# Performance work log

Measured on AMD Instinct MI355X. Metric: run time of the kernel, lower is better.

The kernel has to match this reference:

```python
import jax, jax.numpy as jnp
import numpy as np

B, S = 2, 2048          # batch, seq_len (tokens flattened to T=B*S)
HID = 2048              # hidden_size
H = 16                  # num_heads
DN, DR, DV = 128, 64, 128   # qk_nope_head_dim, qk_rope_head_dim, v_head_dim
QKD = DN + DR           # qk_head_dim = 192
QLR, KVR = 1536, 512    # q_lora_rank, kv_lora_rank
THETA = 10000.0
EPS = 1e-6
SCALE = QKD ** -0.5


def rmsnorm(x, w):
    return x * jax.lax.rsqrt(jnp.mean(x * x, axis=-1, keepdims=True) + EPS) * w


def rope_gptj(x, pos):
    # non-neox (interleaved / GPT-J) style on partial head dim DR
    # x: [T, Hx, DR], pos: [T]
    half = DR // 2
    inv_freq = 1.0 / (THETA ** (jnp.arange(half, dtype=jnp.float32) * 2.0 / DR))
    ang = pos.astype(jnp.float32)[:, None] * inv_freq[None, :]      # [T, half]
    cos = jnp.cos(ang)[:, None, :]
    sin = jnp.sin(ang)[:, None, :]
    x1 = x[..., 0::2]
    x2 = x[..., 1::2]
    o1 = x1 * cos - x2 * sin
    o2 = x2 * cos + x1 * sin
    return jnp.stack([o1, o2], axis=-1).reshape(x.shape)


def setup_inputs() -> dict:
    key = jax.random.key(0)
    ks = jax.random.split(key, 8)
    T = B * S
    positions = jnp.tile(jnp.arange(S, dtype=jnp.int64 if jax.config.jax_enable_x64 else jnp.int32), B)
    hidden_states = jax.random.normal(ks[0], (T, HID), dtype=jnp.float32)
    s = 0.02
    Wqa = jax.random.normal(ks[1], (HID, QLR), dtype=jnp.float32) * s
    q_a_ln_w = jnp.ones((QLR,), dtype=jnp.float32)
    Wqb = jax.random.normal(ks[2], (QLR, H * QKD), dtype=jnp.float32) * s
    Wkva = jax.random.normal(ks[3], (HID, KVR + DR), dtype=jnp.float32) * s
    kv_a_ln_w = jnp.ones((KVR,), dtype=jnp.float32)
    Wkvb = jax.random.normal(ks[4], (KVR, H * (DN + DV)), dtype=jnp.float32) * s
    Wo = jax.random.normal(ks[5], (H * DV, HID), dtype=jnp.float32) * s
    return {"positions": positions, "hidden_states": hidden_states, "Wqa": Wqa,
            "q_a_ln_w": q_a_ln_w, "Wqb": Wqb, "Wkva": Wkva,
            "kv_a_ln_w": kv_a_ln_w, "Wkvb": Wkvb, "Wo": Wo}


def reference(positions, hidden_states, Wqa, q_a_ln_w, Wqb, Wkva, kv_a_ln_w, Wkvb, Wo):
    T = hidden_states.shape[0]
    # --- Q path: low-rank compression ---
    ckq = hidden_states @ Wqa                       # [T, QLR]
    q_c = rmsnorm(ckq, q_a_ln_w)
    q = (q_c @ Wqb).reshape(T, H, QKD)              # [T, H, 192]
    q_nope, q_pe = q[..., :DN], q[..., DN:]
    # --- KV path: latent compression + shared rope key ---
    kv_no_split = hidden_states @ Wkva              # [T, KVR+DR]
    kv_c, k_pe = kv_no_split[:, :KVR], kv_no_split[:, KVR:]
    kv_c_normed = rmsnorm(kv_c, kv_a_ln_w)
    kv = (kv_c_normed @ Wkvb).reshape(T, H, DN + DV)
    k_nope, v = kv[..., :DN], kv[..., DN:]
    # --- RoPE on partial dims (non-neox) ---
    q_pe = rope_gptj(q_pe, positions)               # [T, H, DR]
    k_pe = rope_gptj(k_pe[:, None, :], positions)   # [T, 1, DR]
    # --- assemble full q/k per batch ---
    qf = jnp.concatenate([q_nope, q_pe], axis=-1).reshape(B, S, H, QKD)
    kf = jnp.concatenate([k_nope, jnp.broadcast_to(k_pe, (T, H, DR))], axis=-1).reshape(B, S, H, QKD)
    vf = v.reshape(B, S, H, DV)
    # --- causal attention ---
    scores = jnp.einsum('bqhd,bkhd->bhqk', qf, kf) * SCALE
    mask = jnp.tril(jnp.ones((S, S), dtype=bool))
    scores = jnp.where(mask[None, None], scores, jnp.finfo(scores.dtype).min)
    probs = jax.nn.softmax(scores, axis=-1)
    attn = jnp.einsum('bhqk,bkhd->bqhd', probs, vf).reshape(T, H * DV)
    # --- output projection ---
    return attn @ Wo                                # [T, HID]
```

## Files before the change

### kernel.cpp

```cpp
#include <hip/hip_runtime.h>
#include <hip/hip_bf16.h>

typedef __hip_bfloat16 bf16;
typedef short bf16x8 __attribute__((ext_vector_type(8)));
typedef float f32x4 __attribute__((ext_vector_type(4)));

#define MFMA16(a, b, c) __builtin_amdgcn_mfma_f32_16x16x32_bf16((a), (b), (c), 0, 0, 0)

__device__ __forceinline__ short f2bs(float f) {
  bf16 h = __float2bfloat16(f);
  return __builtin_bit_cast(short, h);
}
__device__ __forceinline__ float bs2f(short s) {
  return __bfloat162float(__builtin_bit_cast(bf16, s));
}

__device__ __forceinline__ void gload16(const void* g, const void* l) {
  __builtin_amdgcn_global_load_lds(
      (const __attribute__((address_space(1))) unsigned int*)g,
      (__attribute__((address_space(3))) unsigned int*)l, 16, 0, 0);
}

__device__ __forceinline__ void t_cvt_core(const float* __restrict__ src,
                                           bf16* __restrict__ dst, int K, int N,
                                           int bx, int by, short Ts[64][72]) {
  const long n0 = (long)bx * 64, k0 = (long)by * 64;
  const int r = threadIdx.x >> 2, c4 = threadIdx.x & 3;
  const float* s = src + (k0 + r) * (long)N + n0 + c4 * 16;
  #pragma unroll
  for (int j = 0; j < 4; ++j) {
    float4 v = *(const float4*)(s + j * 4);
    Ts[r][c4 * 16 + j * 4 + 0] = f2bs(v.x);
    Ts[r][c4 * 16 + j * 4 + 1] = f2bs(v.y);
    Ts[r][c4 * 16 + j * 4 + 2] = f2bs(v.z);
    Ts[r][c4 * 16 + j * 4 + 3] = f2bs(v.w);
  }
  __syncthreads();
  union { uint4 v; short sh[8]; } o0, o1;
  #pragma unroll
  for (int j = 0; j < 8; ++j) o0.sh[j] = Ts[c4 * 16 + j][r];
  #pragma unroll
  for (int j = 0; j < 8; ++j) o1.sh[j] = Ts[c4 * 16 + 8 + j][r];
  *(uint4*)(dst + (n0 + r) * (long)K + k0 + c4 * 16)     = o0.v;
  *(uint4*)(dst + (n0 + r) * (long)K + k0 + c4 * 16 + 8) = o1.v;
}

__global__ __launch_bounds__(256) void prep_all(
    const float* __restrict__ hs_f, bf16* __restrict__ hs_c,
    const float* __restrict__ qln_f, bf16* __restrict__ qln_c,
    const float* __restrict__ kvln_f, bf16* __restrict__ kvln_c,
    const float* __restrict__ Wqa_f, bf16* __restrict__ wqaT,
    const float* __restrict__ Wkva_f, bf16* __restrict__ wkvaT,
    const float* __restrict__ Wqb_f, bf16* __restrict__ wqbT,
    const float* __restrict__ Wkvb_f, bf16* __restrict__ wkvbT,
    const float* __restrict__ Wo_f, bf16* __restrict__ woT)
{
  __shared__ __align__(16) short Ts[64][72];
  const int bid = blockIdx.x;
  if (bid < 4097) {
    int i = bid * 256 + threadIdx.x;
    const float* s; bf16* d; int idx;
    if (i < 1048576)            { s = hs_f;   d = hs_c;   idx = i; }
    else if (i < 1048576 + 192) { s = qln_f;  d = qln_c;  idx = i - 1048576; }
    else                        { s = kvln_f; d = kvln_c; idx = i - 1048768; }
    const float4* sp = (const float4*)s;
    float4 a = sp[2 * idx], b = sp[2 * idx + 1];
    union { uint4 v; short sh[8]; } o;
    o.sh[0] = f2bs(a.x); o.sh[1] = f2bs(a.y); o.sh[2] = f2bs(a.z); o.sh[3] = f2bs(a.w);
    o.sh[4] = f2bs(b.x); o.sh[5] = f2bs(b.y); o.sh[6] = f2bs(b.z); o.sh[7] = f2bs(b.w);
    ((uint4*)d)[idx] = o.v;
  } else if (bid < 4865) {
    int l = bid - 4097;  t_cvt_core(Wqa_f, wqaT, 2048, 1536, l % 24, l / 24, Ts);
  } else if (bid < 5153) {
    int l = bid - 4865;  t_cvt_core(Wkva_f, wkvaT, 2048, 576, l % 9, l / 9, Ts);
  } else if (bid < 6305) {
    int l = bid - 5153;  t_cvt_core(Wqb_f, wqbT, 1536, 3072, l % 48, l / 48, Ts);
  } else if (bid < 6817) {
    int l = bid - 6305;  t_cvt_core(Wkvb_f, wkvbT, 512, 4096, l % 64, l / 64, Ts);
  } else {
    int l = bid - 6817;  t_cvt_core(Wo_f, woT, 2048, 2048, l % 32, l / 32, Ts);
  }
}

template<bool F32OUT>
__device__ __forceinline__ void gemm_core(
    short* As, short* Bs,
    const bf16* __restrict__ A, const bf16* __restrict__ BT, void* __restrict__ Cv,
    int N, int K, int lda, int ldb, int ldc, bf16* __restrict__ C2, int ncut,
    int nx, int nwg, int lin)
{
  const int tid = threadIdx.x, lane = tid & 63, w = tid >> 6;
  const int l15 = lane & 15, l4 = lane >> 4;
  const int wr = w >> 1, wc = w & 1;
  const int sl = (lin & 7) * (nwg >> 3) + (lin >> 3);
  const long bm = (long)(sl / nx) * 128, bn = (long)(sl % nx) * 128;
  f32x4 acc[4][4] = {};

  const int srow = tid >> 3;
  const int scs = (tid & 7) ^ (srow & 7);
  const int rsw = l15 & 7;

  for (int k0 = 0; k0 < K; k0 += 64) {
    __syncthreads();
    #pragma unroll
    for (int j = 0; j < 4; ++j) {
      const unsigned lb = __builtin_amdgcn_readfirstlane((j * 256 + w * 64) * 16);
      gload16(A + (bm + j * 32 + srow) * (long)lda + k0 + scs * 8, (char*)As + lb);
      gload16(BT + (bn + j * 32 + srow) * (long)ldb + k0 + scs * 8, (char*)Bs + lb);
    }
    __syncthreads();
    #pragma unroll
    for (int kk = 0; kk < 2; ++kk) {
      bf16x8 a[4], b[4];
      const int slot = (kk * 4 + l4) ^ rsw;
      #pragma unroll
      for (int mi = 0; mi < 4; ++mi)
        a[mi] = *(const bf16x8*)&As[(wr * 64 + mi * 16 + l15) * 64 + slot * 8];
      #pragma unroll
      for (int ni = 0; ni < 4; ++ni)
        b[ni] = *(const bf16x8*)&Bs[(wc * 64 + ni * 16 + l15) * 64 + slot * 8];
      #pragma unroll
      for (int mi = 0; mi < 4; ++mi)
        #pragma unroll
        for (int ni = 0; ni < 4; ++ni)
          acc[mi][ni] = MFMA16(a[mi], b[ni], acc[mi][ni]);
    }
  }
  #pragma unroll
  for (int mi = 0; mi < 4; ++mi)
    #pragma unroll
    for (int ni = 0; ni < 4; ++ni)
      #pragma unroll
      for (int r = 0; r < 4; ++r) {
        long row = bm + wr * 64 + mi * 16 + l4 * 4 + r;
        long col = bn + wc * 64 + ni * 16 + l15;
        float v = acc[mi][ni][r];
        if (F32OUT) {
          ((float*)Cv)[row * ldc + col] = v;
        } else if (C2 && col >= ncut) {
          C2[row * 640 + (col - ncut)] = __float2bfloat16(v);
        } else {
          ((bf16*)Cv)[row * (long)ldc + col] = __float2bfloat16(v);
        }
      }
}

template<bool F32OUT>
__global__ __launch_bounds__(256) void gemm_v4(
    const bf16* __restrict__ A, const bf16* __restrict__ BT, void* __restrict__ Cv,
    int N, int K, int lda, int ldb, int ldc, bf16* __restrict__ C2, int ncut)
{
  __shared__ __align__(16) short As[128 * 64];
  __shared__ __align__(16) short Bs[128 * 64];
  const int nx = gridDim.x, nwg = nx * gridDim.y;
  const int lin = blockIdx.y * nx + blockIdx.x;
  gemm_core<F32OUT>(As, Bs, A, BT, Cv, N, K, lda, ldb, ldc, C2, ncut, nx, nwg, lin);
}

#define TS_S 139
__global__ __launch_bounds__(256) void gemm_dual(
    const bf16* __restrict__ ckq, const bf16* __restrict__ wqbT, bf16* __restrict__ q,
    const bf16* __restrict__ kvns, const bf16* __restrict__ wkvbT,
    bf16* __restrict__ Kf, bf16* __restrict__ Vt)
{
  __shared__ __align__(16) short LDSU[128 * TS_S];
  short* As = LDSU;
  short* Bs = LDSU + 8192;
  const int bid = blockIdx.x;
  if (bid < 768) {
    gemm_core<false>(As, Bs, ckq, wqbT, q, 3072, 1536, 1536, 1536, 3072, nullptr, 0,
                     24, 768, bid);
    return;
  }
  const int lin = bid - 768;
  const int tid = threadIdx.x, lane = tid & 63, w = tid >> 6;
  const int l15 = lane & 15, l4 = lane >> 4;
  const int wr = w >> 1, wc = w & 1;
  const int sl = (lin & 7) * 128 + (lin >> 3);
  const long bm = (long)(sl / 32) * 128, bn = (long)(sl % 32) * 128;
  f32x4 acc[4][4] = {};
  const int srow = tid >> 3;
  const int scs = (tid & 7) ^ (srow & 7);
  const int rsw = l15 & 7;

  for (int k0 = 0; k0 < 512; k0 += 64) {
    __syncthreads();
    #pragma unroll
    for (int j = 0; j < 4; ++j) {
      const unsigned lb = __builtin_amdgcn_readfirstlane((j * 256 + w * 64) * 16);
      gload16(kvns + (bm + j * 32 + srow) * 640L + k0 + scs * 8, (char*)As + lb);
      gload16(wkvbT + (bn + j * 32 + srow) * 512L + k0 + scs * 8, (char*)Bs + lb);
    }
    __syncthreads();
    #pragma unroll
    for (int kk = 0; kk < 2; ++kk) {
      bf16x8 a[4], b[4];
      const int slot = (kk * 4 + l4) ^ rsw;
      #pragma unroll
      for (int mi = 0; mi < 4; ++mi)
        a[mi] = *(const bf16x8*)&As[(wr * 64 + mi * 16 + l15) * 64 + slot * 8];
      #pragma unroll
      for (int ni = 0; ni < 4; ++ni)
        b[ni] = *(const bf16x8*)&Bs[(wc * 64 + ni * 16 + l15) * 64 + slot * 8];
      #pragma unroll
      for (int mi = 0; mi < 4; ++mi)
        #pragma unroll
        for (int ni = 0; ni < 4; ++ni)
          acc[mi][ni] = MFMA16(a[mi], b[ni], acc[mi][ni]);
    }
  }

  const int h = (int)(bn >> 8);
  const int lc = (int)(bn & 255);
  const int bh = (int)(bm >> 11) * 16 + h;
  const int tsb = (int)(bm & 2047);

  __syncthreads();
  #pragma unroll
  for (int mi = 0; mi < 4; ++mi)
    #pragma unroll
    for (int ni = 0; ni < 4; ++ni)
      #pragma unroll
      for (int r = 0; r < 4; ++r)
        LDSU[(wr * 64 + mi * 16 + l4 * 4 + r) * TS_S + wc * 64 + ni * 16 + l15] =
            f2bs(acc[mi][ni][r]);
  __syncthreads();

  if (lc == 0) {
    #pragma unroll
    for (int j = 0; j < 8; ++j) {
      int u = j * 256 + tid;
      int tl = u >> 4, cs = u & 15;
      union { uint4 v; short sh[8]; } o;
      #pragma unroll
      for (int i = 0; i < 8; ++i) o.sh[i] = LDSU[tl * TS_S + cs * 8 + i];
      *(uint4*)(Kf + ((size_t)bh * 2048 + tsb + tl) * 192 +
                ((cs ^ (tl & 7)) << 3)) = o.v;
    }
  } else {
    #pragma unroll
    for (int j = 0; j < 8; ++j) {
      int u = j * 256 + tid;
      int d = u >> 4, slo = u & 15;
      int k0l = (slo >> 3) << 6;
      int cs = slo & 7;
      int tb = k0l + cs * 8;
      union { uint4 v; short sh[8]; } o;
      #pragma unroll
      for (int i = 0; i < 8; ++i) o.sh[i] = LDSU[(tb + i) * TS_S + d];
      *(uint4*)(Vt + ((size_t)(bh * 128 + d)) * 2048 + tsb + k0l +
                ((cs ^ (d & 7)) << 3)) = o.v;
    }
  }
}

template<int C>
__device__ __forceinline__ void rms_core(bf16* __restrict__ xr,
                                         const bf16* __restrict__ w, float* red)
{
  constexpr int PER = C / 256;
  const int tid = threadIdx.x;
  float v[PER];
  float ss = 0.f;
  #pragma unroll
  for (int k = 0; k < PER; ++k) {
    float f = __bfloat162float(xr[tid + k * 256]);
    v[k] = f; ss += f * f;
  }
  #pragma unroll
  for (int off = 1; off < 64; off <<= 1) ss += __shfl_xor(ss, off);
  if ((tid & 63) == 0) red[tid >> 6] = ss;
  __syncthreads();
  float tot = red[0] + red[1] + red[2] + red[3];
  float scale = rsqrtf(tot / (float)C + 1e-6f);
  #pragma unroll
  for (int k = 0; k < PER; ++k)
    xr[tid + k * 256] =
        __float2bfloat16(v[k] * scale * __bfloat162float(w[tid + k * 256]));
}

__global__ __launch_bounds__(256) void rms_pe_dual(bf16* __restrict__ ckq,
                                                   const bf16* __restrict__ qw,
                                                   bf16* __restrict__ kvns,
                                                   const bf16* __restrict__ kvw,
                                                   bf16* __restrict__ Kf)
{
  __shared__ float red[4];
  __shared__ short pe[64];
  const int bid = blockIdx.x, tid = threadIdx.x;
  if (bid < 4096) {
    rms_core<1536>(ckq + (long)bid * 1536, qw, red);
    return;
  }
  const int t = bid - 4096;
  rms_core<512>(kvns + (long)t * 640, kvw, red);
  if (tid < 32) {
    int i = tid;
    float p = (float)(t & 2047);
    float freq = powf(10000.0f, -(float)i / 32.0f);
    float sn, cs;
    sincosf(p * freq, &sn, &cs);
    float y1 = __bfloat162float(kvns[(long)t * 640 + 512 + 2 * i]);
    float y2 = __bfloat162float(kvns[(long)t * 640 + 512 + 2 * i + 1]);
    pe[2 * i]     = f2bs(y1 * cs - y2 * sn);
    pe[2 * i + 1] = f2bs(y2 * cs + y1 * sn);
  }
  __syncthreads();
  if (tid < 128) {
    const int hh = tid >> 3, j = tid & 7;
    const int swz = t & 7;
    const int b = t >> 11, ts = t & 2047;
    uint4 val = *(const uint4*)&pe[(j ^ swz) * 8];
    *(uint4*)(Kf + ((size_t)(b * 16 + hh) * 2048 + ts) * 192 + (16 + j) * 8) = val;
  }
}

__global__ __launch_bounds__(256) void attn_v7(const bf16* __restrict__ q,
                                               const bf16* __restrict__ Kf,
                                               const bf16* __restrict__ Vt,
                                               bf16* __restrict__ attn)
{
  __shared__ __align__(16) short Ks[2 * 64 * 192];
  __shared__ __align__(16) short Vs[128 * 64];
  __shared__ __align__(16) short Ps[4][16 * 64];
  const float SC2 = 0.10411442245076847f;
  const int tid = threadIdx.x, lane = tid & 63, w = tid >> 6;
  const int l15 = lane & 15, l4 = lane >> 4;
  const int lin = blockIdx.x;
  const int x = lin & 7, j = lin >> 3;
  const int bh = x * 4 + (j >> 4), p = j & 15;
  const int b = bh >> 4, h = bh & 15;
  const unsigned lbase = __builtin_amdgcn_readfirstlane(w * 64 * 16);

  #pragma unroll
  for (int half = 0; half < 2; ++half) {
    const int qt = half ? (31 - p) : p;
    const long qrow0 = (long)b * 2048 + qt * 64;
    const int rowt = qt * 64 + w * 16 + l15;

    bf16x8 qf[6];
    {
      const short* qrow = (const short*)q + (qrow0 + w * 16 + l15) * 3072 + h * 192;
      #pragma unroll
      for (int kc = 0; kc < 6; ++kc)
        qf[kc] = *(const bf16x8*)(qrow + kc * 32 + l4 * 8);
    }
    {
      float pos = (float)rowt;
      #pragma unroll
      for (int kc = 4; kc < 6; ++kc)
        #pragma unroll
        for (int pr = 0; pr < 4; ++pr) {
          int i = (kc - 4) * 16 + l4 * 4 + pr;
          float freq = __expf((float)i * -0.28782313662425572f);
          float sn, cs;
          sincosf(pos * freq, &sn, &cs);
          float x1 = bs2f(qf[kc][2 * pr]), x2 = bs2f(qf[kc][2 * pr + 1]);
          qf[kc][2 * pr]     = f2bs(x1 * cs - x2 * sn);
          qf[kc][2 * pr + 1] = f2bs(x2 * cs + x1 * sn);
        }
    }
    f32x4 o[8] = {};
    float mreg = -1e30f, ls = 0.f;
    const int nch = qt + 1;

    {
      const char* ksrc = (const char*)(Kf + (long)bh * 2048 * 192);
      #pragma unroll
      for (int jj = 0; jj < 6; ++jj)
        gload16(ksrc + (jj * 256 + tid) * 16, (char*)Ks + jj * 4096 + lbase);
    }
    __syncthreads();

    for (int c = 0; c < nch; ++c) {
      const int k0 = c * 64;
      const int cb = (c & 1) * 24576;
      if (c + 1 < nch) {
        const char* ksrc = (const char*)(Kf + ((long)bh * 2048 + k0 + 64) * 192);
        const int nb = ((c + 1) & 1) * 24576;
        #pragma unroll
        for (int jj = 0; jj < 6; ++jj)
          gload16(ksrc + (jj * 256 + tid) * 16, (char*)Ks + nb + jj * 4096 + lbase);
      }
      {
        #pragma unroll
        for (int jj = 0; jj < 4; ++jj) {
          int seg = jj * 256 + tid;
          const bf16* vsrc = Vt + ((long)bh * 128 + (seg >> 3)) * 2048 + k0 + (seg & 7) * 8;
          gload16(vsrc, (char*)Vs + jj * 4096 + lbase);
        }
      }
      __builtin_amdgcn_s_setprio(1);
      f32x4 s[4] = {};
      #pragma unroll
      for (int kc = 0; kc < 6; ++kc)
        #pragma unroll
        for (int kg = 0; kg < 4; ++kg) {
          int row = kg * 16 + l15;
          int slot = (kc * 4 + l4) ^ (l15 & 7);
          bf16x8 kb = *(const bf16x8*)((const char*)Ks + cb + (row * 192 + slot * 8) * 2);
          s[kg] = MFMA16(kb, qf[kc], s[kg]);
        }
      __builtin_amdgcn_s_setprio(0);

      const bool diag = (c == qt);
      float pk[16];
      #pragma unroll
      for (int kg = 0; kg < 4; ++kg)
        #pragma unroll
        for (int r = 0; r < 4; ++r) {
          float v = s[kg][r];
          if (diag && (k0 + kg * 16 + l4 * 4 + r > rowt)) v = -1e30f;
          pk[kg * 4 + r] = v;
        }
      float cm = pk[0];
      #pragma unroll
      for (int i = 1; i < 16; ++i) cm = fmaxf(cm, pk[i]);
      cm = fmaxf(cm, __shfl_xor(cm, 16));
      cm = fmaxf(cm, __shfl_xor(cm, 32));
      cm *= SC2;
      if (__ballot(cm > mreg + 12.0f)) {
        float mn = fmaxf(mreg, cm);
        float al = exp2f(mreg - mn);
        ls *= al;
        float af[4];
        #pragma unroll
        for (int r = 0; r < 4; ++r) af[r] = __shfl(al, l4 * 4 + r);
        #pragma unroll
        for (int f = 0; f < 8; ++f)
          #pragma unroll
          for (int r = 0; r < 4; ++r) o[f][r] *= af[r];
        mreg = mn;
      }
      float ps = 0.f;
      #pragma unroll
      for (int i = 0; i < 16; ++i) {
        pk[i] = exp2f(fmaf(pk[i], SC2, -mreg));
        ps += pk[i];
      }
      ps += __shfl_xor(ps, 16);
      ps += __shfl_xor(ps, 32);
      ls += ps;
      #pragma unroll
      for (int kg = 0; kg < 4; ++kg)
        #pragma unroll
        for (int pr = 0; pr < 2; ++pr) {
          int key2 = kg * 16 + l4 * 4 + pr * 2;
          int sl = (key2 >> 3) ^ (l15 & 7);
          unsigned lo = (unsigned short)f2bs(pk[kg * 4 + pr * 2]);
          unsigned hi = (unsigned short)f2bs(pk[kg * 4 + pr * 2 + 1]);
          *(unsigned*)&Ps[w][l15 * 64 + sl * 8 + (key2 & 7)] = lo | (hi << 16);
        }
      __syncthreads();

      __builtin_amdgcn_s_setprio(1);
      #pragma unroll
      for (int ks = 0; ks < 2; ++ks) {
        int psl = (ks * 4 + l4) ^ (l15 & 7);
        bf16x8 pa = *(const bf16x8*)&Ps[w][l15 * 64 + psl * 8];
        #pragma unroll
        for (int f = 0; f < 8; ++f) {
          int vrow = f * 16 + l15;
          int vsl = (ks * 4 + l4) ^ (l15 & 7);
          bf16x8 bv = *(const bf16x8*)&Vs[vrow * 64 + vsl * 8];
          o[f] = MFMA16(pa, bv, o[f]);
        }
      }
      __builtin_amdgcn_s_setprio(0);
      __syncthreads();
    }

    #pragma unroll
    for (int r = 0; r < 4; ++r) {
      float lsr = __shfl(ls, l4 * 4 + r);
      float inv = 1.0f / lsr;
      long t = qrow0 + w * 16 + l4 * 4 + r;
      bf16* dst = attn + t * 2048 + h * 128;
      #pragma unroll
      for (int f = 0; f < 8; ++f)
        dst[f * 16 + l15] = __float2bfloat16(o[f][r] * inv);
    }
  }
}

extern "C" void kernel_launch(void* const* d_in, const int* in_sizes, int n_in,
                              void* d_out, int out_size, void* d_ws, size_t ws_size,
                              hipStream_t stream) {
  const float* hs_f   = (const float*)d_in[1];
  const float* Wqa_f  = (const float*)d_in[2];
  const float* qln_f  = (const float*)d_in[3];
  const float* Wqb_f  = (const float*)d_in[4];
  const float* Wkva_f = (const float*)d_in[5];
  const float* kvln_f = (const float*)d_in[6];
  const float* Wkvb_f = (const float*)d_in[7];
  const float* Wo_f   = (const float*)d_in[8];

  bf16* base = (bf16*)d_ws;
  bf16* hs_c  = base;
  bf16* wqaT  = base + 8388608;
  bf16* wkvaT = base + 11534336;
  bf16* q     = base;
  bf16* ckq   = base + 12713984;
  bf16* qln_c = base + 19005440;
  bf16* kvln_c= base + 19006976;
  bf16* attnb = base + 12713984;
  bf16* wqbT  = base + 21102592;
  bf16* wkvbT = base + 25821184;
  bf16* woT   = base + 27918336;
  bf16* kvns  = base + 32112640;
  bf16* Kf    = base + 34734080;
  bf16* Vt    = base + 47316992;

  prep_all<<<7841, 256, 0, stream>>>(hs_f, hs_c, qln_f, qln_c, kvln_f, kvln_c,
                                     Wqa_f, wqaT, Wkva_f, wkvaT,
                                     Wqb_f, wqbT, Wkvb_f, wkvbT, Wo_f, woT);
  gemm_v4<false><<<dim3(17, 32), 256, 0, stream>>>(hs_c, wqaT, ckq, 2176, 2048,
                                                   2048, 2048, 1536, kvns, 1536);
  rms_pe_dual<<<8192, 256, 0, stream>>>(ckq, qln_c, kvns, kvln_c, Kf);
  gemm_dual<<<1792, 256, 0, stream>>>(ckq, wqbT, q, kvns, wkvbT, Kf, Vt);
  attn_v7<<<512, 256, 0, stream>>>(q, Kf, Vt, attnb);
  gemm_v4<true><<<dim3(16, 32), 256, 0, stream>>>(attnb, woT, d_out, 2048, 2048,
                                                  2048, 2048, 2048, nullptr, 0);
}
```

Before: 283.0 us.

## Use 256x128 GEMM tiles with 512 threads and drop attention K double-buffering

The GEMM kernels move from 128x128 tiles with 256 threads to 256x128 tiles with 512 threads (8 waves), so each loaded B tile is reused across twice as many rows and the grid is halved. The fused kv_b epilogue now writes its transposed K/V output in two 128-row halves through LDS. The attention kernel goes back to a single K buffer: the next K chunk is prefetched after the softmax barrier instead of double-buffering. This cuts LDS use, but part of the K load latency is exposed again and the ring-buffer race is left to barrier placement.

```diff
diff --git a/kernel.cpp b/kernel.cpp
--- a/kernel.cpp
+++ b/kernel.cpp
@@ -83,17 +83,17 @@
 }
 
 template<bool F32OUT>
-__device__ __forceinline__ void gemm_core(
+__device__ __forceinline__ void gemm_core256(
     short* As, short* Bs,
     const bf16* __restrict__ A, const bf16* __restrict__ BT, void* __restrict__ Cv,
-    int N, int K, int lda, int ldb, int ldc, bf16* __restrict__ C2, int ncut,
+    int K, int lda, int ldb, int ldc, bf16* __restrict__ C2, int ncut,
     int nx, int nwg, int lin)
 {
   const int tid = threadIdx.x, lane = tid & 63, w = tid >> 6;
   const int l15 = lane & 15, l4 = lane >> 4;
   const int wr = w >> 1, wc = w & 1;
   const int sl = (lin & 7) * (nwg >> 3) + (lin >> 3);
-  const long bm = (long)(sl / nx) * 128, bn = (long)(sl % nx) * 128;
+  const long bm = (long)(sl / nx) * 256, bn = (long)(sl % nx) * 128;
   f32x4 acc[4][4] = {};
 
   const int srow = tid >> 3;
@@ -104,9 +104,13 @@
     __syncthreads();
     #pragma unroll
     for (int j = 0; j < 4; ++j) {
-      const unsigned lb = __builtin_amdgcn_readfirstlane((j * 256 + w * 64) * 16);
-      gload16(A + (bm + j * 32 + srow) * (long)lda + k0 + scs * 8, (char*)As + lb);
-      gload16(BT + (bn + j * 32 + srow) * (long)ldb + k0 + scs * 8, (char*)Bs + lb);
+      const unsigned lb = __builtin_amdgcn_readfirstlane((j * 512 + w * 64) * 16);
+      gload16(A + (bm + j * 64 + srow) * (long)lda + k0 + scs * 8, (char*)As + lb);
+    }
+    #pragma unroll
+    for (int j = 0; j < 2; ++j) {
+      const unsigned lb = __builtin_amdgcn_readfirstlane((j * 512 + w * 64) * 16);
+      gload16(BT + (bn + j * 64 + srow) * (long)ldb + k0 + scs * 8, (char*)Bs + lb);
     }
     __syncthreads();
     #pragma unroll
@@ -146,38 +150,38 @@
 }
 
 template<bool F32OUT>
-__global__ __launch_bounds__(256) void gemm_v4(
+__global__ __launch_bounds__(512) void gemm_v5(
     const bf16* __restrict__ A, const bf16* __restrict__ BT, void* __restrict__ Cv,
-    int N, int K, int lda, int ldb, int ldc, bf16* __restrict__ C2, int ncut)
-{
-  __shared__ __align__(16) short As[128 * 64];
+    int K, int lda, int ldb, int ldc, bf16* __restrict__ C2, int ncut)
+{
+  __shared__ __align__(16) short As[256 * 64];
   __shared__ __align__(16) short Bs[128 * 64];
   const int nx = gridDim.x, nwg = nx * gridDim.y;
   const int lin = blockIdx.y * nx + blockIdx.x;
-  gemm_core<F32OUT>(As, Bs, A, BT, Cv, N, K, lda, ldb, ldc, C2, ncut, nx, nwg, lin);
+  gemm_core256<F32OUT>(As, Bs, A, BT, Cv, K, lda, ldb, ldc, C2, ncut, nx, nwg, lin);
 }
 
 #define TS_S 139
-__global__ __launch_bounds__(256) void gemm_dual(
+__global__ __launch_bounds__(512) void gemm_dual(
     const bf16* __restrict__ ckq, const bf16* __restrict__ wqbT, bf16* __restrict__ q,
     const bf16* __restrict__ kvns, const bf16* __restrict__ wkvbT,
     bf16* __restrict__ Kf, bf16* __restrict__ Vt)
 {
-  __shared__ __align__(16) short LDSU[128 * TS_S];
+  __shared__ __align__(16) short LDSU[256 * 64 + 128 * 64];
   short* As = LDSU;
-  short* Bs = LDSU + 8192;
+  short* Bs = LDSU + 256 * 64;
   const int bid = blockIdx.x;
-  if (bid < 768) {
-    gemm_core<false>(As, Bs, ckq, wqbT, q, 3072, 1536, 1536, 1536, 3072, nullptr, 0,
-                     24, 768, bid);
+  if (bid < 384) {
+    gemm_core256<false>(As, Bs, ckq, wqbT, q, 1536, 1536, 1536, 3072, nullptr, 0,
+                        24, 384, bid);
     return;
   }
-  const int lin = bid - 768;
+  const int lin = bid - 384;
   const int tid = threadIdx.x, lane = tid & 63, w = tid >> 6;
   const int l15 = lane & 15, l4 = lane >> 4;
   const int wr = w >> 1, wc = w & 1;
-  const int sl = (lin & 7) * 128 + (lin >> 3);
-  const long bm = (long)(sl / 32) * 128, bn = (long)(sl % 32) * 128;
+  const int sl = (lin & 7) * 64 + (lin >> 3);
+  const long bm = (long)(sl / 32) * 256, bn = (long)(sl % 32) * 128;
   f32x4 acc[4][4] = {};
   const int srow = tid >> 3;
   const int scs = (tid & 7) ^ (srow & 7);
@@ -187,9 +191,13 @@
     __syncthreads();
     #pragma unroll
     for (int j = 0; j < 4; ++j) {
-      const unsigned lb = __builtin_amdgcn_readfirstlane((j * 256 + w * 64) * 16);
-      gload16(kvns + (bm + j * 32 + srow) * 640L + k0 + scs * 8, (char*)As + lb);
-      gload16(wkvbT + (bn + j * 32 + srow) * 512L + k0 + scs * 8, (char*)Bs + lb);
+      const unsigned lb = __builtin_amdgcn_readfirstlane((j * 512 + w * 64) * 16);
+      gload16(kvns + (bm + j * 64 + srow) * 640L + k0 + scs * 8, (char*)As + lb);
+    }
+    #pragma unroll
+    for (int j = 0; j < 2; ++j) {
+      const unsigned lb = __builtin_amdgcn_readfirstlane((j * 512 + w * 64) * 16);
+      gload16(wkvbT + (bn + j * 64 + srow) * 512L + k0 + scs * 8, (char*)Bs + lb);
     }
     __syncthreads();
     #pragma unroll
@@ -215,41 +223,45 @@
   const int bh = (int)(bm >> 11) * 16 + h;
   const int tsb = (int)(bm & 2047);
 
-  __syncthreads();
-  #pragma unroll
-  for (int mi = 0; mi < 4; ++mi)
-    #pragma unroll
-    for (int ni = 0; ni < 4; ++ni)
-      #pragma unroll
-      for (int r = 0; r < 4; ++r)
-        LDSU[(wr * 64 + mi * 16 + l4 * 4 + r) * TS_S + wc * 64 + ni * 16 + l15] =
-            f2bs(acc[mi][ni][r]);
-  __syncthreads();
-
-  if (lc == 0) {
-    #pragma unroll
-    for (int j = 0; j < 8; ++j) {
-      int u = j * 256 + tid;
-      int tl = u >> 4, cs = u & 15;
-      union { uint4 v; short sh[8]; } o;
-      #pragma unroll
-      for (int i = 0; i < 8; ++i) o.sh[i] = LDSU[tl * TS_S + cs * 8 + i];
-      *(uint4*)(Kf + ((size_t)bh * 2048 + tsb + tl) * 192 +
-                ((cs ^ (tl & 7)) << 3)) = o.v;
-    }
-  } else {
-    #pragma unroll
-    for (int j = 0; j < 8; ++j) {
-      int u = j * 256 + tid;
-      int d = u >> 4, slo = u & 15;
-      int k0l = (slo >> 3) << 6;
-      int cs = slo & 7;
-      int tb = k0l + cs * 8;
-      union { uint4 v; short sh[8]; } o;
-      #pragma unroll
-      for (int i = 0; i < 8; ++i) o.sh[i] = LDSU[(tb + i) * TS_S + d];
-      *(uint4*)(Vt + ((size_t)(bh * 128 + d)) * 2048 + tsb + k0l +
-                ((cs ^ (d & 7)) << 3)) = o.v;
+  #pragma unroll
+  for (int hf = 0; hf < 2; ++hf) {
+    __syncthreads();
+    if ((wr >> 1) == hf) {
+      #pragma unroll
+      for (int mi = 0; mi < 4; ++mi)
+        #pragma unroll
+        for (int ni = 0; ni < 4; ++ni)
+          #pragma unroll
+          for (int r = 0; r < 4; ++r)
+            LDSU[((wr & 1) * 64 + mi * 16 + l4 * 4 + r) * TS_S +
+                 wc * 64 + ni * 16 + l15] = f2bs(acc[mi][ni][r]);
+    }
+    __syncthreads();
+    if (lc == 0) {
+      #pragma unroll
+      for (int j = 0; j < 4; ++j) {
+        int u = j * 512 + tid;
+        int tl = u >> 4, cs = u & 15;
+        union { uint4 v; short sh[8]; } o;
+        #pragma unroll
+        for (int i = 0; i < 8; ++i) o.sh[i] = LDSU[tl * TS_S + cs * 8 + i];
+        int t = tsb + hf * 128 + tl;
+        *(uint4*)(Kf + ((size_t)bh * 2048 + t) * 192 + ((cs ^ (t & 7)) << 3)) = o.v;
+      }
+    } else {
+      #pragma unroll
+      for (int j = 0; j < 4; ++j) {
+        int u = j * 512 + tid;
+        int d = u >> 4, slo = u & 15;
+        int k0l = (slo >> 3) << 6;
+        int cs = slo & 7;
+        int tb = k0l + cs * 8;
+        union { uint4 v; short sh[8]; } o;
+        #pragma unroll
+        for (int i = 0; i < 8; ++i) o.sh[i] = LDSU[(tb + i) * TS_S + d];
+        *(uint4*)(Vt + ((size_t)(bh * 128 + d)) * 2048 + tsb + hf * 128 + k0l +
+                  ((cs ^ (d & 7)) << 3)) = o.v;
+      }
     }
   }
 }
@@ -315,12 +327,12 @@
   }
 }
 
-__global__ __launch_bounds__(256) void attn_v7(const bf16* __restrict__ q,
+__global__ __launch_bounds__(256) void attn_v6(const bf16* __restrict__ q,
                                                const bf16* __restrict__ Kf,
                                                const bf16* __restrict__ Vt,
                                                bf16* __restrict__ attn)
 {
-  __shared__ __align__(16) short Ks[2 * 64 * 192];
+  __shared__ __align__(16) short Ks[64 * 192];
   __shared__ __align__(16) short Vs[128 * 64];
   __shared__ __align__(16) short Ps[4][16 * 64];
   const float SC2 = 0.10411442245076847f;
@@ -374,14 +386,6 @@
 
     for (int c = 0; c < nch; ++c) {
       const int k0 = c * 64;
-      const int cb = (c & 1) * 24576;
-      if (c + 1 < nch) {
-        const char* ksrc = (const char*)(Kf + ((long)bh * 2048 + k0 + 64) * 192);
-        const int nb = ((c + 1) & 1) * 24576;
-        #pragma unroll
-        for (int jj = 0; jj < 6; ++jj)
-          gload16(ksrc + (jj * 256 + tid) * 16, (char*)Ks + nb + jj * 4096 + lbase);
-      }
       {
         #pragma unroll
         for (int jj = 0; jj < 4; ++jj) {
@@ -398,7 +402,7 @@
         for (int kg = 0; kg < 4; ++kg) {
           int row = kg * 16 + l15;
           int slot = (kc * 4 + l4) ^ (l15 & 7);
-          bf16x8 kb = *(const bf16x8*)((const char*)Ks + cb + (row * 192 + slot * 8) * 2);
+          bf16x8 kb = *(const bf16x8*)&Ks[row * 192 + slot * 8];
           s[kg] = MFMA16(kb, qf[kc], s[kg]);
         }
       __builtin_amdgcn_s_setprio(0);
@@ -452,6 +456,13 @@
           *(unsigned*)&Ps[w][l15 * 64 + sl * 8 + (key2 & 7)] = lo | (hi << 16);
         }
       __syncthreads();
+
+      if (c + 1 < nch) {
+        const char* ksrc = (const char*)(Kf + ((long)bh * 2048 + k0 + 64) * 192);
+        #pragma unroll
+        for (int jj = 0; jj < 6; ++jj)
+          gload16(ksrc + (jj * 256 + tid) * 16, (char*)Ks + jj * 4096 + lbase);
+      }
 
       __builtin_amdgcn_s_setprio(1);
       #pragma unroll
@@ -514,11 +525,11 @@
   prep_all<<<7841, 256, 0, stream>>>(hs_f, hs_c, qln_f, qln_c, kvln_f, kvln_c,
                                      Wqa_f, wqaT, Wkva_f, wkvaT,
                                      Wqb_f, wqbT, Wkvb_f, wkvbT, Wo_f, woT);
-  gemm_v4<false><<<dim3(17, 32), 256, 0, stream>>>(hs_c, wqaT, ckq, 2176, 2048,
+  gemm_v5<false><<<dim3(17, 16), 512, 0, stream>>>(hs_c, wqaT, ckq, 2048,
                                                    2048, 2048, 1536, kvns, 1536);
   rms_pe_dual<<<8192, 256, 0, stream>>>(ckq, qln_c, kvns, kvln_c, Kf);
-  gemm_dual<<<1792, 256, 0, stream>>>(ckq, wqbT, q, kvns, wkvbT, Kf, Vt);
-  attn_v7<<<512, 256, 0, stream>>>(q, Kf, Vt, attnb);
-  gemm_v4<true><<<dim3(16, 32), 256, 0, stream>>>(attnb, woT, d_out, 2048, 2048,
+  gemm_dual<<<896, 512, 0, stream>>>(ckq, wqbT, q, kvns, wkvbT, Kf, Vt);
+  attn_v6<<<512, 256, 0, stream>>>(q, Kf, Vt, attnb);
+  gemm_v5<true><<<dim3(16, 16), 512, 0, stream>>>(attnb, woT, d_out, 2048,
                                                   2048, 2048, 2048, nullptr, 0);
 }
```

New measurement: 296.3 us. 4.7% more time.
